# Kernel tuning notes

Measured on AMD Instinct MI355X. Metric: run time of the kernel, lower is better.

## Reference

```python
import jax, jax.numpy as jnp
import numpy as np

B, H, W = 8, 64, 64
DIM, HEADS, WS = 512, 8, 8
C2 = DIM // 2            # attention branch channels
HD = C2 // HEADS         # head dim = 32
NH, NW = H // WS, W // WS
WIN = WS * WS            # tokens per window = 64
SCALE = HD ** -0.5
EPS = 1e-5


def layer_norm(x, g, b):
    m = jnp.mean(x, axis=-1, keepdims=True)
    v = jnp.mean((x - m) ** 2, axis=-1, keepdims=True)
    return (x - m) * jax.lax.rsqrt(v + EPS) * g + b


def dwconv3x3(x, w, b=None):
    # x: (N, C, h, w); w: (C, 1, 3, 3) depthwise
    out = jax.lax.conv_general_dilated(
        x, w, window_strides=(1, 1), padding='SAME',
        feature_group_count=x.shape[1],
        dimension_numbers=('NCHW', 'OIHW', 'NCHW'))
    if b is not None:
        out = out + b[None, :, None, None]
    return out


def setup_inputs() -> dict:
    key = jax.random.key(0)
    ks = jax.random.split(key, 8)
    r = lambda k, s: (jax.random.normal(k, s, jnp.float32) * 0.02)
    return {
        'x': jax.random.normal(ks[0], (B, H * W, DIM), jnp.float32),
        'norm1_g': jnp.ones((DIM,), jnp.float32),
        'norm1_b': jnp.zeros((DIM,), jnp.float32),
        'qkv_w': r(ks[1], (C2, 3 * C2)),
        'qkv_b': jnp.zeros((3 * C2,), jnp.float32),
        'lepe_w': r(ks[2], (C2, 1, 3, 3)),
        'lepe_b': jnp.zeros((C2,), jnp.float32),
        'convloc_w': r(ks[3], (C2, 1, 3, 3)),
        'proj_w': r(ks[4], (DIM, DIM)),
        'proj_b': jnp.zeros((DIM,), jnp.float32),
        'norm2_g': jnp.ones((DIM,), jnp.float32),
        'norm2_b': jnp.zeros((DIM,), jnp.float32),
        'fc1_w': r(ks[5], (DIM, 4 * DIM)),
        'fc1_b': jnp.zeros((4 * DIM,), jnp.float32),
        'fc2_w': r(ks[6], (4 * DIM, DIM)),
        'fc2_b': jnp.zeros((DIM,), jnp.float32),
    }


def reference(x, norm1_g, norm1_b, qkv_w, qkv_b, lepe_w, lepe_b, convloc_w,
              proj_w, proj_b, norm2_g, norm2_b, fc1_w, fc1_b, fc2_w, fc2_b):
    img = layer_norm(x, norm1_g, norm1_b)                      # (B, L, DIM)

    # qkv from first half of channels
    qkv = img[..., :C2] @ qkv_w + qkv_b                        # (B, L, 3*C2)
    qkv = qkv.reshape(B, H * W, 3, C2)
    q, k, v = qkv[:, :, 0], qkv[:, :, 1], qkv[:, :, 2]

    def win6(t):  # (B, L, C2) -> (B, NH, NW, WS, WS, C2)
        return t.reshape(B, NH, WS, NW, WS, C2).transpose(0, 1, 3, 2, 4, 5)

    def to_heads(t6):
        return t6.reshape(-1, WIN, HEADS, HD).transpose(0, 2, 1, 3)

    qh = to_heads(win6(q)) * SCALE
    kh = to_heads(win6(k))

    # v + LePE: depthwise 3x3 conv applied per-window
    vw = win6(v).transpose(0, 1, 2, 5, 3, 4).reshape(-1, C2, WS, WS)
    lepe = dwconv3x3(vw, lepe_w, lepe_b)                       # (nWin, C2, WS, WS)
    vh = vw.reshape(-1, HEADS, HD, WIN).transpose(0, 1, 3, 2)
    leh = lepe.reshape(-1, HEADS, HD, WIN).transpose(0, 1, 3, 2)

    attn = jax.nn.softmax(jnp.einsum('nhqd,nhkd->nhqk', qh, kh), axis=-1)
    o = jnp.einsum('nhqk,nhkd->nhqd', attn, vh) + leh

    # merge windows back to (B, L, C2)
    o = o.transpose(0, 2, 1, 3).reshape(B, NH, NW, WS, WS, C2)
    o = o.transpose(0, 1, 3, 2, 4, 5).reshape(B, H * W, C2)

    # parallel depthwise-conv branch on second half of channels (no bias)
    x2 = img[..., C2:].transpose(0, 2, 1).reshape(B, C2, H, W)
    x2 = dwconv3x3(x2, convloc_w)
    x2 = x2.reshape(B, C2, H * W).transpose(0, 2, 1)

    local = jnp.concatenate([o, x2], axis=-1) @ proj_w + proj_b
    x = x + local

    # MLP_FFN: Linear -> GELU -> Linear
    h = jax.nn.gelu(layer_norm(x, norm2_g, norm2_b) @ fc1_w + fc1_b,
                    approximate=False)
    x = x + (h @ fc2_w + fc2_b)
    return x
```

## Files before the change

kernel.cpp:

```cpp
#include <hip/hip_runtime.h>
#include <cstdint>
#include <cstddef>

typedef unsigned short u16;
typedef __attribute__((ext_vector_type(8))) short short8;
typedef __attribute__((ext_vector_type(4))) float f32x4;

#define DIM 512
#define C2  256
#define HD  32
#define SCALE_Q 0.17677669529663689f

__device__ __forceinline__ float bf2f(u16 u){ return __uint_as_float(((unsigned)u) << 16); }
__device__ __forceinline__ u16 f2bf(float f){
  unsigned u = __float_as_uint(f);
  unsigned r = (u + 0x7FFFu + ((u >> 16) & 1u)) >> 16;
  return (u16)r;
}

__device__ __forceinline__ f32x4 mfma16(short8 a, short8 b, f32x4 c){
  return __builtin_amdgcn_mfma_f32_16x16x32_bf16(a, b, c, 0, 0, 0);
}

__device__ __forceinline__ void gload16(const u16* g, u16* l){
  __builtin_amdgcn_global_load_lds((const __attribute__((address_space(1))) void*)g,
                                   (__attribute__((address_space(3))) void*)l, 16, 0, 0);
}

__device__ __forceinline__ float gelu_f(float v){
  float e = __expf(-1.702f * v);
  return v * __builtin_amdgcn_rcpf(1.0f + e);
}

__global__ __launch_bounds__(256) void transpose_kernel(const float* __restrict__ W,
                                                        u16* __restrict__ WT, int K, int N){
  __shared__ u16 Tl[32][33];
  int n0 = blockIdx.x * 32, k0 = blockIdx.y * 32;
  int tx = threadIdx.x & 31, ty = threadIdx.x >> 5;
#pragma unroll
  for (int i = 0; i < 4; i++){
    int k = ty * 4 + i;
    Tl[k][tx] = f2bf(W[(size_t)(k0 + k) * N + n0 + tx]);
  }
  __syncthreads();
#pragma unroll
  for (int i = 0; i < 4; i++){
    int n = ty * 4 + i;
    WT[(size_t)(n0 + n) * K + k0 + tx] = Tl[tx][n];
  }
}

__global__ __launch_bounds__(256) void ln_kernel(const float* __restrict__ x, const float* __restrict__ g,
                                                 const float* __restrict__ bta, u16* __restrict__ out){
  int row  = blockIdx.x * 4 + (threadIdx.x >> 6);
  int lane = threadIdx.x & 63;
  size_t base = (size_t)row * DIM + lane * 8;
  float4 v0 = *(const float4*)(x + base);
  float4 v1 = *(const float4*)(x + base + 4);
  float f[8] = {v0.x, v0.y, v0.z, v0.w, v1.x, v1.y, v1.z, v1.w};
  float s = 0.f;
#pragma unroll
  for (int j = 0; j < 8; j++) s += f[j];
#pragma unroll
  for (int m = 1; m < 64; m <<= 1) s += __shfl_xor(s, m, 64);
  float mean = s * (1.0f / DIM);
  float vs = 0.f;
#pragma unroll
  for (int j = 0; j < 8; j++){ float d = f[j] - mean; vs += d * d; }
#pragma unroll
  for (int m = 1; m < 64; m <<= 1) vs += __shfl_xor(vs, m, 64);
  float rstd = rsqrtf(vs * (1.0f / DIM) + 1e-5f);
  float4 g0 = *(const float4*)(g + lane * 8);
  float4 g1 = *(const float4*)(g + lane * 8 + 4);
  float4 b0 = *(const float4*)(bta + lane * 8);
  float4 b1 = *(const float4*)(bta + lane * 8 + 4);
  float gg[8] = {g0.x, g0.y, g0.z, g0.w, g1.x, g1.y, g1.z, g1.w};
  float bb[8] = {b0.x, b0.y, b0.z, b0.w, b1.x, b1.y, b1.z, b1.w};
  short8 o;
#pragma unroll
  for (int j = 0; j < 8; j++){
    float r = (f[j] - mean) * rstd * gg[j] + bb[j];
    o[j] = (short)f2bf(r);
  }
  *(short8*)(out + base) = o;
}

template<int EPI, bool OUT_BF16>
__global__ __launch_bounds__(512, 2) void gemm8_kernel(
    const u16* __restrict__ A, int lda,
    const u16* __restrict__ WT,
    const float* __restrict__ bias,
    const float* R, int ldr,
    void* Cv, int ldc, int K)
{
  __shared__ u16 Al[2][2][256 * 32];
  __shared__ u16 Bl[2][2][256 * 32];
  const int tid = threadIdx.x;
  const int l   = tid & 63;
  const int w   = tid >> 6;
  const int wr  = w >> 2;
  const int wc  = w & 3;
  const int l16 = l & 15, lhi = l >> 4;

  const int gx = gridDim.x;
  int bid = blockIdx.y * gx + blockIdx.x;
  int nwg = gx * gridDim.y;
  int sw  = (nwg & 7) ? bid : ((bid & 7) * (nwg >> 3) + (bid >> 3));
  const int col0 = (sw % gx) * 256, row0 = (sw / gx) * 256;
  const int NT = K >> 6;

  const int srow = w * 16 + (l >> 2);
  const int cs   = (((l & 3) ^ ((l >> 3) & 3)) * 8);
  const u16* pA = A  + (size_t)(row0 + srow) * lda + cs;
  const u16* pB = WT + (size_t)(col0 + srow) * K  + cs;
  const size_t a128 = (size_t)128 * lda, b128 = (size_t)128 * K;

  auto stageA = [&](int tt, int hh){
    if (tt < NT){
      size_t go = (size_t)tt * 64 + (size_t)hh * 32;
      gload16(pA + go,        &Al[tt & 1][hh][(w * 16) * 32]);
      gload16(pA + a128 + go, &Al[tt & 1][hh][(128 + w * 16) * 32]);
    }
  };
  auto stageB = [&](int tt, int hh){
    if (tt < NT){
      size_t go = (size_t)tt * 64 + (size_t)hh * 32;
      gload16(pB + go,        &Bl[tt & 1][hh][(w * 16) * 32]);
      gload16(pB + b128 + go, &Bl[tt & 1][hh][(128 + w * 16) * 32]);
    }
  };

  const int rdo = l16 * 32 + (lhi ^ ((l16 >> 1) & 3)) * 8;

  f32x4 acc[8][4] = {};
  short8 af[4], bf[4];

  stageA(0, 0); stageB(0, 0); stageA(0, 1); stageB(0, 1); stageA(1, 0); stageB(1, 0);
  asm volatile("s_waitcnt vmcnt(4)" ::: "memory");
  __builtin_amdgcn_sched_barrier(0);
  __builtin_amdgcn_s_barrier();

#define PHASE(BC, KH, QM, STAGES) do{                                                   \
    if ((QM) == 0){                                                                     \
      _Pragma("unroll")                                                                 \
      for (int n = 0; n < 4; n++)                                                       \
        bf[n] = *(const short8*)&Bl[BC][KH][(wc * 64 + n * 16) * 32 + rdo];             \
    }                                                                                   \
    _Pragma("unroll")                                                                   \
    for (int m = 0; m < 4; m++)                                                         \
      af[m] = *(const short8*)&Al[BC][KH][(wr * 128 + (QM) * 64 + m * 16) * 32 + rdo];  \
    STAGES;                                                                             \
    __builtin_amdgcn_s_barrier();                                                       \
    asm volatile("s_waitcnt lgkmcnt(0)" ::: "memory");                                  \
    __builtin_amdgcn_sched_barrier(0);                                                  \
    __builtin_amdgcn_s_setprio(1);                                                      \
    _Pragma("unroll")                                                                   \
    for (int m = 0; m < 4; m++)                                                         \
      _Pragma("unroll")                                                                 \
      for (int n = 0; n < 4; n++)                                                       \
        acc[(QM) * 4 + m][n] = mfma16(bf[n], af[m], acc[(QM) * 4 + m][n]);              \
    __builtin_amdgcn_s_setprio(0);                                                      \
    __builtin_amdgcn_s_barrier();                                                       \
  }while(0)

  for (int t = 0; t < NT; t++){
    const int bc = t & 1;
    PHASE(bc, 0, 0, stageA(t + 1, 1));
    PHASE(bc, 0, 1, stageB(t + 1, 1));
    PHASE(bc, 1, 0, stageA(t + 2, 0));
    PHASE(bc, 1, 1, stageB(t + 2, 0));
    if (t + 2 < NT) asm volatile("s_waitcnt vmcnt(4)" ::: "memory");
    else            asm volatile("s_waitcnt vmcnt(0)" ::: "memory");
    __builtin_amdgcn_sched_barrier(0);
    __builtin_amdgcn_s_barrier();
  }
#undef PHASE

  float4 bvs[4];
#pragma unroll
  for (int n = 0; n < 4; n++)
    bvs[n] = *(const float4*)&bias[col0 + wc * 64 + n * 16 + lhi * 4];
#pragma unroll
  for (int mq = 0; mq < 8; mq++){
    int grow = row0 + wr * 128 + mq * 16 + l16;
#pragma unroll
    for (int n = 0; n < 4; n++){
      int gcol = col0 + wc * 64 + n * 16 + lhi * 4;
      float4 vv = { acc[mq][n][0] + bvs[n].x, acc[mq][n][1] + bvs[n].y,
                    acc[mq][n][2] + bvs[n].z, acc[mq][n][3] + bvs[n].w };
      if constexpr (EPI == 1){
        float4 rv = *(const float4*)&R[(size_t)grow * ldr + gcol];
        vv.x += rv.x; vv.y += rv.y; vv.z += rv.z; vv.w += rv.w;
      }
      if constexpr (EPI == 2){
        vv.x = gelu_f(vv.x); vv.y = gelu_f(vv.y); vv.z = gelu_f(vv.z); vv.w = gelu_f(vv.w);
      }
      if constexpr (OUT_BF16){
        ushort4 o4 = { f2bf(vv.x), f2bf(vv.y), f2bf(vv.z), f2bf(vv.w) };
        *(ushort4*)&((u16*)Cv)[(size_t)grow * ldc + gcol] = o4;
      } else {
        *(float4*)&((float*)Cv)[(size_t)grow * ldc + gcol] = vv;
      }
    }
  }
}

__global__ __launch_bounds__(64) void attn_kernel(
    const u16* __restrict__ qkv, const float* __restrict__ lw,
    const float* __restrict__ lb, u16* __restrict__ out)
{
  __shared__ float Ks[64][33];
  __shared__ float Vs[64][33];
  __shared__ float Wle[32][9];
  __shared__ float Lb[32];
  int head = blockIdx.x & 7, win = blockIdx.x >> 3;
  int wx = win & 7, wy = (win >> 3) & 7, b = win >> 6;
  int l  = threadIdx.x;
  int py = l >> 3, px = l & 7;
  size_t t = (size_t)b * 4096 + (size_t)(wy * 8 + py) * 64 + (wx * 8 + px);
  const u16* base = qkv + t * 768 + head * HD;

  float q[32];
#pragma unroll
  for (int j = 0; j < 32; j += 8){
    short8 vq = *(const short8*)(base + j);
    short8 vk = *(const short8*)(base + 256 + j);
    short8 vv = *(const short8*)(base + 512 + j);
#pragma unroll
    for (int e = 0; e < 8; e++){
      q[j + e]     = bf2f((u16)vq[e]) * SCALE_Q;
      Ks[l][j + e] = bf2f((u16)vk[e]);
      Vs[l][j + e] = bf2f((u16)vv[e]);
    }
  }
  for (int i = l; i < 288; i += 64) Wle[i / 9][i % 9] = lw[(head * 32 + i / 9) * 9 + (i % 9)];
  if (l < 32) Lb[l] = lb[head * 32 + l];
  __syncthreads();

  float sc[64];
  float mx = -1e30f;
#pragma unroll
  for (int k = 0; k < 64; k++){
    float s = 0.f;
#pragma unroll
    for (int d = 0; d < 32; d++) s += q[d] * Ks[k][d];
    sc[k] = s; mx = fmaxf(mx, s);
  }
  float sum = 0.f;
#pragma unroll
  for (int k = 0; k < 64; k++){ float e = __expf(sc[k] - mx); sc[k] = e; sum += e; }
  float inv = 1.0f / sum;
  float o[32];
#pragma unroll
  for (int d = 0; d < 32; d++) o[d] = 0.f;
#pragma unroll
  for (int k = 0; k < 64; k++){
    float p = sc[k] * inv;
#pragma unroll
    for (int d = 0; d < 32; d++) o[d] += p * Vs[k][d];
  }
#pragma unroll
  for (int ky = 0; ky < 3; ky++){
    int yy = py + ky - 1;
    if (yy < 0 || yy >= 8) continue;
#pragma unroll
    for (int kx = 0; kx < 3; kx++){
      int xx = px + kx - 1;
      if (xx < 0 || xx >= 8) continue;
      int kp = yy * 8 + xx;
#pragma unroll
      for (int d = 0; d < 32; d++) o[d] += Wle[d][ky * 3 + kx] * Vs[kp][d];
    }
  }
  u16* op = out + t * DIM + head * HD;
#pragma unroll
  for (int d = 0; d < 32; d += 4){
    ushort4 o4 = { f2bf(o[d] + Lb[d]), f2bf(o[d + 1] + Lb[d + 1]),
                   f2bf(o[d + 2] + Lb[d + 2]), f2bf(o[d + 3] + Lb[d + 3]) };
    *(ushort4*)&op[d] = o4;
  }
}

__global__ __launch_bounds__(256) void convloc_kernel(const u16* __restrict__ img,
    const float* __restrict__ w, u16* __restrict__ out){
  int c  = threadIdx.x;
  int pg = blockIdx.x;
  int b  = pg >> 8;
  int p0 = (pg & 255) * 16;
  float wt[9];
#pragma unroll
  for (int i = 0; i < 9; i++) wt[i] = w[c * 9 + i];
  for (int pi = 0; pi < 16; pi++){
    int p = p0 + pi;
    int y = p >> 6, x = p & 63;
    float acc = 0.f;
#pragma unroll
    for (int ky = 0; ky < 3; ky++){
      int yy = y + ky - 1;
      if (yy < 0 || yy >= 64) continue;
#pragma unroll
      for (int kx = 0; kx < 3; kx++){
        int xx = x + kx - 1;
        if (xx < 0 || xx >= 64) continue;
        acc += wt[ky * 3 + kx] * bf2f(img[((size_t)b * 4096 + yy * 64 + xx) * DIM + C2 + c]);
      }
    }
    out[((size_t)b * 4096 + p) * DIM + C2 + c] = f2bf(acc);
  }
}

extern "C" void kernel_launch(void* const* d_in, const int* in_sizes, int n_in,
                              void* d_out, int out_size, void* d_ws, size_t ws_size,
                              hipStream_t stream){
  const float* x      = (const float*)d_in[0];
  const float* n1g    = (const float*)d_in[1];
  const float* n1b    = (const float*)d_in[2];
  const float* qkv_w  = (const float*)d_in[3];
  const float* qkv_b  = (const float*)d_in[4];
  const float* lepe_w = (const float*)d_in[5];
  const float* lepe_b = (const float*)d_in[6];
  const float* conv_w = (const float*)d_in[7];
  const float* proj_w = (const float*)d_in[8];
  const float* proj_b = (const float*)d_in[9];
  const float* n2g    = (const float*)d_in[10];
  const float* n2b    = (const float*)d_in[11];
  const float* fc1_w  = (const float*)d_in[12];
  const float* fc1_b  = (const float*)d_in[13];
  const float* fc2_w  = (const float*)d_in[14];
  const float* fc2_b  = (const float*)d_in[15];
  float* out = (float*)d_out;

  char* ws = (char*)d_ws;
  u16* img     = (u16*)(ws + 0);
  u16* qkvb    = (u16*)(ws + 33554432ull);
  u16* localb  = (u16*)(ws + 83886080ull);
  u16* y       = (u16*)(ws + 0);
  u16* h       = (u16*)(ws + 33554432ull);
  u16* qkv_wT  = (u16*)(ws + 167772160ull);
  u16* proj_wT = (u16*)(ws + 167772160ull + 393216ull);
  u16* fc1_wT  = (u16*)(ws + 167772160ull + 393216ull + 524288ull);
  u16* fc2_wT  = (u16*)(ws + 167772160ull + 393216ull + 524288ull + 2097152ull);
  float* xa    = (float*)d_out;

  { dim3 g(24, 8);  transpose_kernel<<<g, 256, 0, stream>>>(qkv_w,  qkv_wT,  256, 768);  }
  { dim3 g(16, 16); transpose_kernel<<<g, 256, 0, stream>>>(proj_w, proj_wT, 512, 512);  }
  { dim3 g(64, 16); transpose_kernel<<<g, 256, 0, stream>>>(fc1_w,  fc1_wT,  512, 2048); }
  { dim3 g(16, 64); transpose_kernel<<<g, 256, 0, stream>>>(fc2_w,  fc2_wT,  2048, 512); }

  ln_kernel<<<8192, 256, 0, stream>>>(x, n1g, n1b, img);

  dim3 gq(3, 128);
  gemm8_kernel<0, true><<<gq, 512, 0, stream>>>(img, DIM, qkv_wT, qkv_b, nullptr, 0, qkvb, 768, 256);

  attn_kernel<<<4096, 64, 0, stream>>>(qkvb, lepe_w, lepe_b, localb);
  convloc_kernel<<<2048, 256, 0, stream>>>(img, conv_w, localb);

  dim3 gp(2, 128);
  gemm8_kernel<1, false><<<gp, 512, 0, stream>>>(localb, DIM, proj_wT, proj_b, x, DIM, xa, DIM, 512);

  ln_kernel<<<8192, 256, 0, stream>>>(xa, n2g, n2b, y);

  dim3 g1(8, 128);
  gemm8_kernel<2, true><<<g1, 512, 0, stream>>>(y, DIM, fc1_wT, fc1_b, nullptr, 0, h, 2048, 512);

  dim3 g2(2, 128);
  gemm8_kernel<1, false><<<g2, 512, 0, stream>>>(h, 2048, fc2_wT, fc2_b, xa, DIM, out, DIM, 2048);
}
```

Measured before the change: 449.3 us.

## Replace 256x256 phased GEMM with simpler 128x128 double-buffered GEMM

The GEMM kernel moves from 256x256 tiles with 512 threads and a four-phase, hand-scheduled k-loop to 128x128 tiles with 256 threads and a plain double-buffered loop over 32-wide k-steps. Each GEMM gets its own wrapper kernel and a grid with four times as many blocks. The intent is to cut LDS use and raise occupancy and tail balance. In exchange, data reuse per block drops, global and LDS traffic per flop rises, barriers become more frequent, and the finely interleaved load/MFMA schedule is lost.

```diff
diff --git a/kernel.cpp b/kernel.cpp
--- a/kernel.cpp
+++ b/kernel.cpp
@@ -86,108 +86,87 @@
 }
 
 template<int EPI, bool OUT_BF16>
-__global__ __launch_bounds__(512, 2) void gemm8_kernel(
+__device__ __forceinline__ void gemm_body(
     const u16* __restrict__ A, int lda,
     const u16* __restrict__ WT,
     const float* __restrict__ bias,
     const float* R, int ldr,
     void* Cv, int ldc, int K)
 {
-  __shared__ u16 Al[2][2][256 * 32];
-  __shared__ u16 Bl[2][2][256 * 32];
+  __shared__ u16 Al[2][128 * 32];
+  __shared__ u16 Bl[2][128 * 32];
   const int tid = threadIdx.x;
   const int l   = tid & 63;
   const int w   = tid >> 6;
-  const int wr  = w >> 2;
-  const int wc  = w & 3;
+  const int wr  = w >> 1;
+  const int wc  = w & 1;
   const int l16 = l & 15, lhi = l >> 4;
 
   const int gx = gridDim.x;
   int bid = blockIdx.y * gx + blockIdx.x;
   int nwg = gx * gridDim.y;
   int sw  = (nwg & 7) ? bid : ((bid & 7) * (nwg >> 3) + (bid >> 3));
-  const int col0 = (sw % gx) * 256, row0 = (sw / gx) * 256;
-  const int NT = K >> 6;
-
-  const int srow = w * 16 + (l >> 2);
+  const int col0 = (sw % gx) * 128, row0 = (sw / gx) * 128;
+  const int NT = K >> 5;
+
+  const int srow = w * 32 + (l >> 2);
   const int cs   = (((l & 3) ^ ((l >> 3) & 3)) * 8);
   const u16* pA = A  + (size_t)(row0 + srow) * lda + cs;
   const u16* pB = WT + (size_t)(col0 + srow) * K  + cs;
-  const size_t a128 = (size_t)128 * lda, b128 = (size_t)128 * K;
-
-  auto stageA = [&](int tt, int hh){
+  const size_t a16 = (size_t)16 * lda, b16 = (size_t)16 * K;
+
+  auto stage = [&](int tt){
     if (tt < NT){
-      size_t go = (size_t)tt * 64 + (size_t)hh * 32;
-      gload16(pA + go,        &Al[tt & 1][hh][(w * 16) * 32]);
-      gload16(pA + a128 + go, &Al[tt & 1][hh][(128 + w * 16) * 32]);
+      size_t go = (size_t)tt * 32;
+      u16* la = &Al[tt & 1][(w * 32) * 32];
+      u16* lb = &Bl[tt & 1][(w * 32) * 32];
+      gload16(pA + go,       la);
+      gload16(pA + go + a16, la + 16 * 32);
+      gload16(pB + go,       lb);
+      gload16(pB + go + b16, lb + 16 * 32);
     }
   };
-  auto stageB = [&](int tt, int hh){
-    if (tt < NT){
-      size_t go = (size_t)tt * 64 + (size_t)hh * 32;
-      gload16(pB + go,        &Bl[tt & 1][hh][(w * 16) * 32]);
-      gload16(pB + b128 + go, &Bl[tt & 1][hh][(128 + w * 16) * 32]);
-    }
-  };
 
   const int rdo = l16 * 32 + (lhi ^ ((l16 >> 1) & 3)) * 8;
 
-  f32x4 acc[8][4] = {};
-  short8 af[4], bf[4];
-
-  stageA(0, 0); stageB(0, 0); stageA(0, 1); stageB(0, 1); stageA(1, 0); stageB(1, 0);
-  asm volatile("s_waitcnt vmcnt(4)" ::: "memory");
-  __builtin_amdgcn_sched_barrier(0);
-  __builtin_amdgcn_s_barrier();
-
-#define PHASE(BC, KH, QM, STAGES) do{                                                   \
-    if ((QM) == 0){                                                                     \
-      _Pragma("unroll")                                                                 \
-      for (int n = 0; n < 4; n++)                                                       \
-        bf[n] = *(const short8*)&Bl[BC][KH][(wc * 64 + n * 16) * 32 + rdo];             \
-    }                                                                                   \
-    _Pragma("unroll")                                                                   \
-    for (int m = 0; m < 4; m++)                                                         \
-      af[m] = *(const short8*)&Al[BC][KH][(wr * 128 + (QM) * 64 + m * 16) * 32 + rdo];  \
-    STAGES;                                                                             \
-    __builtin_amdgcn_s_barrier();                                                       \
-    asm volatile("s_waitcnt lgkmcnt(0)" ::: "memory");                                  \
-    __builtin_amdgcn_sched_barrier(0);                                                  \
-    __builtin_amdgcn_s_setprio(1);                                                      \
-    _Pragma("unroll")                                                                   \
-    for (int m = 0; m < 4; m++)                                                         \
-      _Pragma("unroll")                                                                 \
-      for (int n = 0; n < 4; n++)                                                       \
-        acc[(QM) * 4 + m][n] = mfma16(bf[n], af[m], acc[(QM) * 4 + m][n]);              \
-    __builtin_amdgcn_s_setprio(0);                                                      \
-    __builtin_amdgcn_s_barrier();                                                       \
-  }while(0)
+  f32x4 acc[4][4] = {};
+
+  stage(0);
+  __syncthreads();
 
   for (int t = 0; t < NT; t++){
-    const int bc = t & 1;
-    PHASE(bc, 0, 0, stageA(t + 1, 1));
-    PHASE(bc, 0, 1, stageB(t + 1, 1));
-    PHASE(bc, 1, 0, stageA(t + 2, 0));
-    PHASE(bc, 1, 1, stageB(t + 2, 0));
-    if (t + 2 < NT) asm volatile("s_waitcnt vmcnt(4)" ::: "memory");
-    else            asm volatile("s_waitcnt vmcnt(0)" ::: "memory");
+    stage(t + 1);
     __builtin_amdgcn_sched_barrier(0);
-    __builtin_amdgcn_s_barrier();
-  }
-#undef PHASE
+    const int cur = t & 1;
+    short8 af[4], bf[4];
+#pragma unroll
+    for (int n = 0; n < 4; n++)
+      bf[n] = *(const short8*)&Bl[cur][(wc * 64 + n * 16) * 32 + rdo];
+#pragma unroll
+    for (int m = 0; m < 4; m++)
+      af[m] = *(const short8*)&Al[cur][(wr * 64 + m * 16) * 32 + rdo];
+    __builtin_amdgcn_s_setprio(1);
+#pragma unroll
+    for (int m = 0; m < 4; m++)
+#pragma unroll
+      for (int n = 0; n < 4; n++)
+        acc[m][n] = mfma16(bf[n], af[m], acc[m][n]);
+    __builtin_amdgcn_s_setprio(0);
+    __syncthreads();
+  }
 
   float4 bvs[4];
 #pragma unroll
   for (int n = 0; n < 4; n++)
     bvs[n] = *(const float4*)&bias[col0 + wc * 64 + n * 16 + lhi * 4];
 #pragma unroll
-  for (int mq = 0; mq < 8; mq++){
-    int grow = row0 + wr * 128 + mq * 16 + l16;
+  for (int m = 0; m < 4; m++){
+    int grow = row0 + wr * 64 + m * 16 + l16;
 #pragma unroll
     for (int n = 0; n < 4; n++){
       int gcol = col0 + wc * 64 + n * 16 + lhi * 4;
-      float4 vv = { acc[mq][n][0] + bvs[n].x, acc[mq][n][1] + bvs[n].y,
-                    acc[mq][n][2] + bvs[n].z, acc[mq][n][3] + bvs[n].w };
+      float4 vv = { acc[m][n][0] + bvs[n].x, acc[m][n][1] + bvs[n].y,
+                    acc[m][n][2] + bvs[n].z, acc[m][n][3] + bvs[n].w };
       if constexpr (EPI == 1){
         float4 rv = *(const float4*)&R[(size_t)grow * ldr + gcol];
         vv.x += rv.x; vv.y += rv.y; vv.z += rv.z; vv.w += rv.w;
@@ -203,6 +182,23 @@
       }
     }
   }
+}
+
+__global__ __launch_bounds__(256) void gemm_qkv_kernel(const u16* A, int lda, const u16* WT,
+    const float* bias, const float* R, int ldr, void* Cv, int ldc, int K){
+  gemm_body<0, true>(A, lda, WT, bias, R, ldr, Cv, ldc, K);
+}
+__global__ __launch_bounds__(256) void gemm_proj_kernel(const u16* A, int lda, const u16* WT,
+    const float* bias, const float* R, int ldr, void* Cv, int ldc, int K){
+  gemm_body<1, false>(A, lda, WT, bias, R, ldr, Cv, ldc, K);
+}
+__global__ __launch_bounds__(256) void gemm_fc1_kernel(const u16* A, int lda, const u16* WT,
+    const float* bias, const float* R, int ldr, void* Cv, int ldc, int K){
+  gemm_body<2, true>(A, lda, WT, bias, R, ldr, Cv, ldc, K);
+}
+__global__ __launch_bounds__(256) void gemm_fc2_kernel(const u16* A, int lda, const u16* WT,
+    const float* bias, const float* R, int ldr, void* Cv, int ldc, int K){
+  gemm_body<1, false>(A, lda, WT, bias, R, ldr, Cv, ldc, K);
 }
 
 __global__ __launch_bounds__(64) void attn_kernel(
@@ -349,20 +345,20 @@
 
   ln_kernel<<<8192, 256, 0, stream>>>(x, n1g, n1b, img);
 
-  dim3 gq(3, 128);
-  gemm8_kernel<0, true><<<gq, 512, 0, stream>>>(img, DIM, qkv_wT, qkv_b, nullptr, 0, qkvb, 768, 256);
+  dim3 gq(6, 256);
+  gemm_qkv_kernel<<<gq, 256, 0, stream>>>(img, DIM, qkv_wT, qkv_b, nullptr, 0, qkvb, 768, 256);
 
   attn_kernel<<<4096, 64, 0, stream>>>(qkvb, lepe_w, lepe_b, localb);
   convloc_kernel<<<2048, 256, 0, stream>>>(img, conv_w, localb);
 
-  dim3 gp(2, 128);
-  gemm8_kernel<1, false><<<gp, 512, 0, stream>>>(localb, DIM, proj_wT, proj_b, x, DIM, xa, DIM, 512);
+  dim3 gp(4, 256);
+  gemm_proj_kernel<<<gp, 256, 0, stream>>>(localb, DIM, proj_wT, proj_b, x, DIM, xa, DIM, 512);
 
   ln_kernel<<<8192, 256, 0, stream>>>(xa, n2g, n2b, y);
 
-  dim3 g1(8, 128);
-  gemm8_kernel<2, true><<<g1, 512, 0, stream>>>(y, DIM, fc1_wT, fc1_b, nullptr, 0, h, 2048, 512);
-
-  dim3 g2(2, 128);
-  gemm8_kernel<1, false><<<g2, 512, 0, stream>>>(h, 2048, fc2_wT, fc2_b, xa, DIM, out, DIM, 2048);
-}
+  dim3 g1(16, 256);
+  gemm_fc1_kernel<<<g1, 256, 0, stream>>>(y, DIM, fc1_wT, fc1_b, nullptr, 0, h, 2048, 512);
+
+  dim3 g2(4, 256);
+  gemm_fc2_kernel<<<g2, 256, 0, stream>>>(h, 2048, fc2_wT, fc2_b, xa, DIM, out, DIM, 2048);
+}
```

After: 493.0 us. 1.1x slower.
